# Performance work log

Hardware: AMD Instinct MI355X
Metric: run time of the kernel (lower is better)

The kernel has to match this reference:

```python
import jax, jax.numpy as jnp
import numpy as np

B, T, L, M = 64, 2000, 400, 80
SIGMA_FACTOR = 0.05
SIGMA_CAP = 10.0
SIGMA_MIN = 1.5
WARMUP_STEPS = 10000
GLOBAL_STEP = 0  # fresh loss module -> progress = 0
ENTROPY_TARGET = 3.5
ATTN_W_START = 1.0
ATTN_W_MIN = 0.2
EPS = 1e-8


def setup_inputs() -> dict:
    key = jax.random.key(0)
    ks = jax.random.split(key, 8)
    mel_out_postnet = jax.random.normal(ks[0], (B, T, M), jnp.float32)
    mel_out = jax.random.normal(ks[1], (B, T, M), jnp.float32)
    gate_out = jax.random.normal(ks[2], (B, T), jnp.float32)
    # alignments: stacked per-step attention, row-normalized like real softmax outputs
    a = jax.random.uniform(ks[3], (B, T, L), jnp.float32)
    alignments = a / jnp.sum(a, axis=-1, keepdims=True)
    mel_target = jax.random.normal(ks[4], (B, T, M), jnp.float32)
    gate_target = jnp.round(jax.random.uniform(ks[5], (B, T), jnp.float32))
    mel_lengths = jax.random.randint(ks[6], (B,), T // 2, T + 1, jnp.int32).at[0].set(T)
    text_lengths = jax.random.randint(ks[7], (B,), L // 2, L + 1, jnp.int32).at[0].set(L)
    return {
        "mel_out_postnet": mel_out_postnet, "mel_out": mel_out, "gate_out": gate_out,
        "alignments": alignments, "mel_target": mel_target, "gate_target": gate_target,
        "mel_lengths": mel_lengths, "text_lengths": text_lengths,
    }


def _diagonal_target(text_lengths):
    # sigma per batch element; global_step=0 -> progress=0 -> sigma = init_sigma
    init_sigma = jnp.clip(text_lengths.astype(jnp.float32) * SIGMA_FACTOR, 3.0, SIGMA_CAP)
    progress = min(1.0, GLOBAL_STEP / float(WARMUP_STEPS))
    sigma = init_sigma - (init_sigma - SIGMA_MIN) * progress  # [B]
    t = jnp.arange(T, dtype=jnp.int32)  # decoder steps
    Lb = text_lengths[:, None]  # [B,1]
    # expected_pos = min(int(t*Lb/T), Lb-1); positive ints -> integer floor div matches trunc
    exp_pos = jnp.minimum((t[None, :] * Lb) // T, Lb - 1).astype(jnp.float32)  # [B,T]
    pos = jnp.arange(L, dtype=jnp.float32)  # [L]
    z = (pos[None, None, :] - exp_pos[:, :, None]) / sigma[:, None, None]
    g = jnp.exp(-0.5 * z * z)  # [B,T,L]
    valid = (pos[None, None, :] < text_lengths[:, None, None].astype(jnp.float32))
    g = g * valid
    return g / (jnp.sum(g, axis=-1, keepdims=True) + EPS)


def reference(mel_out_postnet, mel_out, gate_out, alignments, mel_target,
              gate_target, mel_lengths, text_lengths):
    # masked L1 on mel (mel_target already [B,T,M], matching the torch transpose)
    valid = (jnp.arange(T)[None, :] < mel_lengths[:, None])[:, :, None]  # [B,T,1]
    vf = valid.astype(jnp.float32)
    n_valid = jnp.sum(vf) * M
    mel_loss_1 = jnp.sum(jnp.abs(mel_out - mel_target) * vf) / n_valid
    mel_loss_2 = jnp.sum(jnp.abs(mel_out_postnet - mel_target) * vf) / n_valid
    loss_mel = mel_loss_1 + mel_loss_2

    # BCEWithLogits, mean reduction (stable form)
    x, z_t = gate_out, gate_target
    loss_gate = jnp.mean(jnp.maximum(x, 0.0) - x * z_t + jnp.log1p(jnp.exp(-jnp.abs(x))))

    # guided-attention KL against diagonal Gaussian target
    target = _diagonal_target(text_lengths)  # [B,T,L]
    attn_safe = jnp.maximum(alignments, EPS)
    log_pred = jnp.log(attn_safe)
    kl_pw = jnp.where(target > 0.0, target * (jnp.log(jnp.maximum(target, EPS)) - log_pred), 0.0)
    attention_kl = jnp.sum(kl_pw) / B / T  # batchmean then / T_dec
    attention_kl = jnp.minimum(attention_kl, 150.0)

    # entropy-gated attention weight (python-float in torch -> stop_gradient)
    attn_entropy = jnp.mean(-jnp.sum(attn_safe * log_pred, axis=2))
    ratio = jnp.maximum(attn_entropy / ENTROPY_TARGET, 0.0)
    weight = jnp.where(attn_entropy <= ENTROPY_TARGET,
                       jnp.maximum(ATTN_W_MIN, ATTN_W_START * ratio),
                       ATTN_W_START)
    weight = jax.lax.stop_gradient(weight)

    total_loss = loss_mel + loss_gate + weight * attention_kl
    return (total_loss, loss_mel, loss_gate, attention_kl)
```

## Files before the change

kernel.cpp:

```cpp
#include <hip/hip_runtime.h>
#include <cstddef>
#include <cstdint>

#define B_ 64
#define T_ 2000
#define L_ 400
#define M_ 80
#define EPSF 1e-8f
#define LOG_EPSF -18.420680743952367f

#define NBLK 2048

__device__ inline float waveReduce(float v) {
#pragma unroll
  for (int m = 32; m >= 1; m >>= 1) v += __shfl_xor(v, m, 64);
  return v;
}

__global__ __launch_bounds__(256) void fused_kernel(
    const float4* __restrict__ mo, const float4* __restrict__ mp,
    const float4* __restrict__ mt, const float* __restrict__ gx,
    const float* __restrict__ gz, const float* __restrict__ align,
    const int* __restrict__ mel_lengths, const int* __restrict__ text_lengths,
    double* __restrict__ ws) {
  const int tid = blockIdx.x * 256 + threadIdx.x;
  const int nthreads = NBLK * 256;

  float mel_acc = 0.f;
  const int N4 = B_ * T_ * (M_ / 4);
  for (int i = tid; i < N4; i += nthreads) {
    int row = i / (M_ / 4);
    int b = row / T_;
    int t = row - b * T_;
    if (t < mel_lengths[b]) {
      float4 a = mo[i], c = mp[i], d = mt[i];
      mel_acc += fabsf(a.x - d.x) + fabsf(a.y - d.y) + fabsf(a.z - d.z) + fabsf(a.w - d.w)
               + fabsf(c.x - d.x) + fabsf(c.y - d.y) + fabsf(c.z - d.z) + fabsf(c.w - d.w);
    }
  }

  float gate_acc = 0.f;
  for (int i = tid; i < B_ * T_; i += nthreads) {
    float xv = gx[i], z = gz[i];
    gate_acc += fmaxf(xv, 0.f) - xv * z + log1pf(__expf(-fabsf(xv)));
  }

  const int lane = threadIdx.x & 63;
  const int wib = threadIdx.x >> 6;
  const int waveId = blockIdx.x * 4 + wib;
  const int numWaves = NBLK * 4;
  float kl_acc = 0.f, ent_acc = 0.f;
  for (int p = waveId; p < B_ * T_; p += numWaves) {
    int b = p / T_;
    int t = p - b * T_;
    int Lb = text_lengths[b];
    float sigma = fminf(fmaxf((float)Lb * 0.05f, 3.0f), 10.0f);
    float invsig = 1.0f / sigma;
    int epi = t * Lb / T_;
    int lim = Lb - 1;
    if (epi > lim) epi = lim;
    float ep = (float)epi;
    const float* row = align + (size_t)p * L_;
    float g[7], lp[7], ee[7];
    float S = 0.f;
#pragma unroll
    for (int k = 0; k < 7; ++k) {
      int l = lane + 64 * k;
      g[k] = 0.f; lp[k] = 0.f; ee[k] = 0.f;
      if (l < L_) {
        float a = row[l];
        float as = fmaxf(a, EPSF);
        float lpv = __logf(as);
        lp[k] = lpv;
        ent_acc -= as * lpv;
        float z = ((float)l - ep) * invsig;
        float e = -0.5f * z * z;
        ee[k] = e;
        float gv = (l < Lb) ? __expf(e) : 0.f;
        g[k] = gv;
        S += gv;
      }
    }
    S = waveReduce(S);
    float Se = S + EPSF;
    float inv = 1.0f / Se;
    float logSe = __logf(Se);
#pragma unroll
    for (int k = 0; k < 7; ++k) {
      int l = lane + 64 * k;
      if (l < L_ && g[k] > 0.f) {
        float tgt = g[k] * inv;
        float lt = fmaxf(ee[k] - logSe, LOG_EPSF);
        kl_acc += tgt * (lt - lp[k]);
      }
    }
  }

  float w0 = waveReduce(mel_acc);
  float w1 = waveReduce(gate_acc);
  float w2 = waveReduce(kl_acc);
  float w3 = waveReduce(ent_acc);
  __shared__ double sh[4][4];
  if (lane == 0) {
    sh[wib][0] = (double)w0; sh[wib][1] = (double)w1;
    sh[wib][2] = (double)w2; sh[wib][3] = (double)w3;
  }
  __syncthreads();
  if (threadIdx.x == 0) {
    ws[blockIdx.x]            = sh[0][0] + sh[1][0] + sh[2][0] + sh[3][0];
    ws[NBLK + blockIdx.x]     = sh[0][1] + sh[1][1] + sh[2][1] + sh[3][1];
    ws[2 * NBLK + blockIdx.x] = sh[0][2] + sh[1][2] + sh[2][2] + sh[3][2];
    ws[3 * NBLK + blockIdx.x] = sh[0][3] + sh[1][3] + sh[2][3] + sh[3][3];
  }
}

__device__ double segSum(const double* __restrict__ p, int n, double* sh) {
  double a = 0.0;
  for (int i = threadIdx.x; i < n; i += 256) a += p[i];
  sh[threadIdx.x] = a;
  __syncthreads();
  for (int s = 128; s > 0; s >>= 1) {
    if ((int)threadIdx.x < s) sh[threadIdx.x] += sh[threadIdx.x + s];
    __syncthreads();
  }
  double r = sh[0];
  __syncthreads();
  return r;
}

__global__ __launch_bounds__(256) void finalize_kernel(
    const double* __restrict__ ws, const int* __restrict__ mel_lengths,
    float* __restrict__ out) {
  __shared__ double sh[256];
  double mel_sum  = segSum(ws, NBLK, sh);
  double gate_sum = segSum(ws + NBLK, NBLK, sh);
  double kl_sum   = segSum(ws + 2 * NBLK, NBLK, sh);
  double ent_sum  = segSum(ws + 3 * NBLK, NBLK, sh);
  if (threadIdx.x == 0) {
    long nv = 0;
    for (int b = 0; b < B_; ++b) nv += mel_lengths[b];
    double n_valid = (double)nv * (double)M_;
    float loss_mel  = (float)(mel_sum / n_valid);
    float loss_gate = (float)(gate_sum / (double)(B_ * T_));
    float kl  = (float)(kl_sum / (double)(B_ * T_));
    kl = fminf(kl, 150.0f);
    float ent = (float)(ent_sum / (double)(B_ * T_));
    float ratio = fmaxf(ent / 3.5f, 0.0f);
    float weight = (ent <= 3.5f) ? fmaxf(0.2f, 1.0f * ratio) : 1.0f;
    out[0] = loss_mel + loss_gate + weight * kl;
    out[1] = loss_mel;
    out[2] = loss_gate;
    out[3] = kl;
  }
}

extern "C" void kernel_launch(void* const* d_in, const int* in_sizes, int n_in,
                              void* d_out, int out_size, void* d_ws, size_t ws_size,
                              hipStream_t stream) {
  const float* mel_out_postnet = (const float*)d_in[0];
  const float* mel_out         = (const float*)d_in[1];
  const float* gate_out        = (const float*)d_in[2];
  const float* alignments      = (const float*)d_in[3];
  const float* mel_target      = (const float*)d_in[4];
  const float* gate_target     = (const float*)d_in[5];
  const int*   mel_lengths     = (const int*)d_in[6];
  const int*   text_lengths    = (const int*)d_in[7];
  float* out = (float*)d_out;
  double* ws = (double*)d_ws;

  fused_kernel<<<dim3(NBLK), dim3(256), 0, stream>>>(
      (const float4*)mel_out, (const float4*)mel_out_postnet,
      (const float4*)mel_target, gate_out, gate_target,
      alignments, mel_lengths, text_lengths, ws);
  finalize_kernel<<<dim3(1), dim3(256), 0, stream>>>(ws, mel_lengths, out);
}
```

Before: 389.1 us.

## Vectorize attention rows with float4 prefetch and interleave phase order across blocks

The attention KL loop now reads each 400-element row as float4 loads, 64 plus 36 lanes, and prefetches the next row while computing the current one. The KL sum is rewritten algebraically as inv*(sum g*lt - sum g*lp), so fewer values stay in registers. Length arrays are staged in shared memory. Odd blocks run the attention phase first while even blocks run the mel/gate phase first, so the different access patterns overlap across the device. The prefetch raises register pressure, and the regrouped sum slightly changes floating-point rounding.

```diff
diff --git a/kernel.cpp b/kernel.cpp
--- a/kernel.cpp
+++ b/kernel.cpp
@@ -10,8 +10,13 @@
 #define LOG_EPSF -18.420680743952367f
 
 #define NBLK 2048
-
-__device__ inline float waveReduce(float v) {
+#define BT_ (B_ * T_)
+#define NTHREADS (NBLK * 256)
+#define NWAVES (NBLK * 4)
+#define L4_ (L_ / 4)
+#define TAIL_LANES (L4_ - 64)
+
+__device__ __forceinline__ float waveReduce(float v) {
 #pragma unroll
   for (int m = 32; m >= 1; m >>= 1) v += __shfl_xor(v, m, 64);
   return v;
@@ -23,78 +28,132 @@
     const float* __restrict__ gz, const float* __restrict__ align,
     const int* __restrict__ mel_lengths, const int* __restrict__ text_lengths,
     double* __restrict__ ws) {
+  __shared__ int sh_ml[B_];
+  __shared__ int sh_tl[B_];
+  if (threadIdx.x < B_) {
+    sh_ml[threadIdx.x] = mel_lengths[threadIdx.x];
+    sh_tl[threadIdx.x] = text_lengths[threadIdx.x];
+  }
+  __syncthreads();
+
   const int tid = blockIdx.x * 256 + threadIdx.x;
-  const int nthreads = NBLK * 256;
-
-  float mel_acc = 0.f;
-  const int N4 = B_ * T_ * (M_ / 4);
-  for (int i = tid; i < N4; i += nthreads) {
-    int row = i / (M_ / 4);
-    int b = row / T_;
-    int t = row - b * T_;
-    if (t < mel_lengths[b]) {
-      float4 a = mo[i], c = mp[i], d = mt[i];
-      mel_acc += fabsf(a.x - d.x) + fabsf(a.y - d.y) + fabsf(a.z - d.z) + fabsf(a.w - d.w)
-               + fabsf(c.x - d.x) + fabsf(c.y - d.y) + fabsf(c.z - d.z) + fabsf(c.w - d.w);
-    }
-  }
-
-  float gate_acc = 0.f;
-  for (int i = tid; i < B_ * T_; i += nthreads) {
-    float xv = gx[i], z = gz[i];
-    gate_acc += fmaxf(xv, 0.f) - xv * z + log1pf(__expf(-fabsf(xv)));
-  }
-
   const int lane = threadIdx.x & 63;
   const int wib = threadIdx.x >> 6;
   const int waveId = blockIdx.x * 4 + wib;
-  const int numWaves = NBLK * 4;
-  float kl_acc = 0.f, ent_acc = 0.f;
-  for (int p = waveId; p < B_ * T_; p += numWaves) {
-    int b = p / T_;
-    int t = p - b * T_;
-    int Lb = text_lengths[b];
-    float sigma = fminf(fmaxf((float)Lb * 0.05f, 3.0f), 10.0f);
-    float invsig = 1.0f / sigma;
-    int epi = t * Lb / T_;
-    int lim = Lb - 1;
-    if (epi > lim) epi = lim;
-    float ep = (float)epi;
-    const float* row = align + (size_t)p * L_;
-    float g[7], lp[7], ee[7];
-    float S = 0.f;
-#pragma unroll
-    for (int k = 0; k < 7; ++k) {
-      int l = lane + 64 * k;
-      g[k] = 0.f; lp[k] = 0.f; ee[k] = 0.f;
-      if (l < L_) {
-        float a = row[l];
-        float as = fmaxf(a, EPSF);
-        float lpv = __logf(as);
-        lp[k] = lpv;
-        ent_acc -= as * lpv;
-        float z = ((float)l - ep) * invsig;
+
+  float mel_acc = 0.f, gate_acc = 0.f, kl_acc = 0.f, ent_acc = 0.f;
+
+  auto do_melgate = [&]() {
+    const int N4 = B_ * T_ * (M_ / 4);
+#pragma unroll 2
+    for (int i = tid; i < N4; i += NTHREADS) {
+      int row = i / (M_ / 4);
+      int b = row / T_;
+      int t = row - b * T_;
+      if (t < sh_ml[b]) {
+        float4 a = mo[i], c = mp[i], d = mt[i];
+        mel_acc += fabsf(a.x - d.x) + fabsf(a.y - d.y) + fabsf(a.z - d.z) + fabsf(a.w - d.w)
+                 + fabsf(c.x - d.x) + fabsf(c.y - d.y) + fabsf(c.z - d.z) + fabsf(c.w - d.w);
+      }
+    }
+    for (int i = tid; i < BT_; i += NTHREADS) {
+      float xv = gx[i], z = gz[i];
+      gate_acc += fmaxf(xv, 0.f) - xv * z + log1pf(__expf(-fabsf(xv)));
+    }
+  };
+
+  auto do_attn = [&]() {
+    const float4* a4 = reinterpret_cast<const float4*>(align);
+    int p = waveId;
+    float4 c0, c1 = make_float4(0.f, 0.f, 0.f, 0.f);
+    if (p < BT_) {
+      const float4* r = a4 + (size_t)p * L4_;
+      c0 = r[lane];
+      if (lane < TAIL_LANES) c1 = r[64 + lane];
+    }
+    while (p < BT_) {
+      const int pn = p + NWAVES;
+      float4 n0, n1;
+      if (pn < BT_) {
+        const float4* r = a4 + (size_t)pn * L4_;
+        n0 = r[lane];
+        if (lane < TAIL_LANES) n1 = r[64 + lane];
+      }
+      int b = p / T_;
+      int t = p - b * T_;
+      int Lb = sh_tl[b];
+      float sigma = fminf(fmaxf((float)Lb * 0.05f, 3.0f), 10.0f);
+      float invsig = 1.0f / sigma;
+      int epi = t * Lb / T_;
+      int lim = Lb - 1;
+      if (epi > lim) epi = lim;
+      float ep = (float)epi;
+
+      float S = 0.f, W = 0.f;
+      float g0[4], g1[4];
+      const int l0 = 4 * lane;
+      const float fl0 = (float)l0;
+      {
+        const float av[4] = {c0.x, c0.y, c0.z, c0.w};
+#pragma unroll
+        for (int j = 0; j < 4; ++j) {
+          float as = fmaxf(av[j], EPSF);
+          float lpv = __logf(as);
+          ent_acc -= as * lpv;
+          float z = (fl0 + (float)j - ep) * invsig;
+          float e = -0.5f * z * z;
+          float gv = ((l0 + j) < Lb) ? __expf(e) : 0.f;
+          g0[j] = gv;
+          S += gv;
+          W += gv * lpv;
+        }
+      }
+      const int l1 = 256 + 4 * lane;
+      const float fl1 = (float)l1;
+      if (lane < TAIL_LANES) {
+        const float av[4] = {c1.x, c1.y, c1.z, c1.w};
+#pragma unroll
+        for (int j = 0; j < 4; ++j) {
+          float as = fmaxf(av[j], EPSF);
+          float lpv = __logf(as);
+          ent_acc -= as * lpv;
+          float z = (fl1 + (float)j - ep) * invsig;
+          float e = -0.5f * z * z;
+          float gv = ((l1 + j) < Lb) ? __expf(e) : 0.f;
+          g1[j] = gv;
+          S += gv;
+          W += gv * lpv;
+        }
+      } else {
+#pragma unroll
+        for (int j = 0; j < 4; ++j) g1[j] = 0.f;
+      }
+      float St = waveReduce(S);
+      float Se = St + EPSF;
+      float inv = 1.0f / Se;
+      float logSe = __logf(Se);
+      float K = 0.f;
+#pragma unroll
+      for (int j = 0; j < 4; ++j) {
+        float z = (fl0 + (float)j - ep) * invsig;
         float e = -0.5f * z * z;
-        ee[k] = e;
-        float gv = (l < Lb) ? __expf(e) : 0.f;
-        g[k] = gv;
-        S += gv;
-      }
-    }
-    S = waveReduce(S);
-    float Se = S + EPSF;
-    float inv = 1.0f / Se;
-    float logSe = __logf(Se);
-#pragma unroll
-    for (int k = 0; k < 7; ++k) {
-      int l = lane + 64 * k;
-      if (l < L_ && g[k] > 0.f) {
-        float tgt = g[k] * inv;
-        float lt = fmaxf(ee[k] - logSe, LOG_EPSF);
-        kl_acc += tgt * (lt - lp[k]);
-      }
-    }
-  }
+        float lt = fmaxf(e - logSe, LOG_EPSF);
+        K += g0[j] * lt;
+      }
+#pragma unroll
+      for (int j = 0; j < 4; ++j) {
+        float z = (fl1 + (float)j - ep) * invsig;
+        float e = -0.5f * z * z;
+        float lt = fmaxf(e - logSe, LOG_EPSF);
+        K += g1[j] * lt;
+      }
+      kl_acc += inv * (K - W);
+      p = pn; c0 = n0; c1 = n1;
+    }
+  };
+
+  if (blockIdx.x & 1) { do_attn(); do_melgate(); }
+  else                { do_melgate(); do_attn(); }
 
   float w0 = waveReduce(mel_acc);
   float w1 = waveReduce(gate_acc);
```

After: 392.2 us. No clear change (+0.8%).
